# Performance work log

Hardware: AMD Instinct MI355X
Metric: run time of the kernel (lower is better)

Reference implementation:

```python
import jax, jax.numpy as jnp
import numpy as np


def setup_inputs() -> dict:
    key = jax.random.key(0)
    kx, kb, kc, ka, kd = jax.random.split(key, 5)
    B, L, D, N = 8, 4096, 1024, 128
    x = jax.random.normal(kx, (B, L, D), jnp.float32)
    B_w = jax.random.normal(kb, (N, D), jnp.float32) * 0.01  # nn.Linear(d_model->d_state).weight
    C_w = jax.random.normal(kc, (D, N), jnp.float32)         # nn.Linear(d_state->d_model).weight
    # stable negative log_A (HiPPO init gives -|diag|+0.1 < 0)
    log_A = -jax.random.uniform(ka, (N,), jnp.float32) * 3.0 - 0.1
    D_param = jax.random.normal(kd, (D,), jnp.float32)
    return dict(x=x, B_w=B_w, C_w=C_w, log_A=log_A, D_param=D_param)


def reference(x, B_w, C_w, log_A, D_param):
    # x: (B,L,D); B_w: (N,D); C_w: (D,N); log_A: (N,); D_param: (D,)
    A = jnp.exp(log_A)                                   # (N,) diagonal transition
    x_proj = jnp.einsum('bld,nd->bln', x, B_w)           # B @ x  -> (B,L,N)

    def step(h, u):                                      # h_t = A*h_{t-1} + u_t
        h = A * h + u
        return h, h

    h0 = jnp.zeros((x.shape[0], B_w.shape[0]), x.dtype)  # (B,N)
    _, hs = jax.lax.scan(step, h0, jnp.swapaxes(x_proj, 0, 1))  # hs: (L,B,N)

    y = jnp.einsum('lbn,dn->bld', hs, C_w)               # C @ h -> (B,L,D)
    y = y + x * D_param                                  # skip term D*x

    last = x_proj[:, -1, :]                              # (B,N)
    final_state = jnp.broadcast_to(last.mean(axis=0, keepdims=True), last.shape)
    return y, final_state
```

## Files before the change

### kernel.cpp

```cpp
#include <hip/hip_runtime.h>


typedef _Float16 half8 __attribute__((ext_vector_type(8)));
typedef _Float16 half4 __attribute__((ext_vector_type(4)));
typedef float f32x4 __attribute__((ext_vector_type(4)));

#define BDIM 8
#define LDIM 4096
#define DDIM 1024
#define NDIM 128
#define MTOT (BDIM * LDIM)
#define CHUNK 32
#define NCHUNK (LDIM / CHUNK)
#define TOTCHUNK (BDIM * NCHUNK)

__device__ __forceinline__ void dma16(const void* g, void* l) {
    __builtin_amdgcn_global_load_lds((const __attribute__((address_space(1))) void*)g,
                                     (__attribute__((address_space(3))) void*)l, 16, 0, 0);
}

__global__ __launch_bounds__(256) void prep(const float* __restrict__ x,
                                            const float* __restrict__ Bw,
                                            const float* __restrict__ Cw,
                                            _Float16* __restrict__ Bwh,
                                            _Float16* __restrict__ Cwh,
                                            float* __restrict__ out) {
    const int blk = blockIdx.x;
    const int t = threadIdx.x;
    if (blk < 128) {
        const int n = blk;
        float s = 0.f;
        const float* br = Bw + n * DDIM;
        for (int b = 0; b < BDIM; ++b) {
            const float* xr = x + ((size_t)b * LDIM + (LDIM - 1)) * DDIM;
            for (int k = t; k < DDIM; k += 256)
                s = fmaf(xr[k], br[k], s);
        }
        __shared__ float red[256];
        red[t] = s;
        __syncthreads();
        for (int off = 128; off > 0; off >>= 1) {
            if (t < off) red[t] += red[t + off];
            __syncthreads();
        }
        if (t == 0) {
            float v = red[0] * 0.125f;
            for (int b = 0; b < BDIM; ++b)
                out[(size_t)MTOT * DDIM + b * NDIM + n] = v;
        }
    } else {
        const int base = (blk - 128) * 4096;
#pragma unroll
        for (int j = 0; j < 4; ++j) {
            int e = base + j * 1024 + t * 4;
            const float* src;
            _Float16* dst;
            if (e < 131072) { src = Bw + e; dst = Bwh + e; }
            else            { src = Cw + (e - 131072); dst = Cwh + (e - 131072); }
            float4 v = *reinterpret_cast<const float4*>(src);
            half4 h = { (_Float16)v.x, (_Float16)v.y, (_Float16)v.z, (_Float16)v.w };
            *reinterpret_cast<half4*>(dst) = h;
        }
    }
}

__global__ __launch_bounds__(256, 8) void gemm1(const float* __restrict__ x,
                                                const _Float16* __restrict__ Bwh,
                                                const float* __restrict__ logA,
                                                float* __restrict__ xp,
                                                float* __restrict__ agg) {
    __shared__ _Float16 As[32 * 64];
    __shared__ _Float16 Bs[128 * 64];
    const int t = threadIdx.x;
    const int row0 = blockIdx.x * 32;
    const int wave = t >> 6, lane = t & 63;
    const int wr = (wave >> 1) * 16, wc = (wave & 1) * 64;
    const int lrow = lane & 15, kq = (lane >> 4) * 8;
    const int kc = kq >> 3;

    f32x4 acc[4] = {};

    for (int kk = 0; kk < DDIM; kk += 64) {
#pragma unroll
        for (int inst = 0; inst < 4; ++inst) {
            int s = inst * 256 + t;
            int r = s >> 3;
            int cs = (s & 7) ^ (r & 7);
            dma16(&Bwh[(size_t)r * DDIM + kk + cs * 8], &Bs[(inst * 256 + wave * 64) * 8]);
        }
#pragma unroll
        for (int j = 0; j < 2; ++j) {
            int s = t + 256 * j;
            int r = s >> 4, c4 = s & 15;
            float4 v = *reinterpret_cast<const float4*>(&x[(size_t)(row0 + r) * DDIM + kk + c4 * 4]);
            half4 h = { (_Float16)v.x, (_Float16)v.y, (_Float16)v.z, (_Float16)v.w };
            int pc = (c4 >> 1) ^ (r & 7);
            *reinterpret_cast<half4*>(&As[r * 64 + pc * 8 + (c4 & 1) * 4]) = h;
        }
        __syncthreads();

        const int arow = wr + lrow;
#pragma unroll
        for (int ks = 0; ks < 2; ++ks) {
            half8 af = *reinterpret_cast<const half8*>(&As[arow * 64 + ((ks * 4 + kc) ^ (arow & 7)) * 8]);
            half8 bf[4];
#pragma unroll
            for (int ct = 0; ct < 4; ++ct) {
                int brow = wc + ct * 16 + lrow;
                bf[ct] = *reinterpret_cast<const half8*>(&Bs[brow * 64 + ((ks * 4 + kc) ^ (brow & 7)) * 8]);
            }
#pragma unroll
            for (int ct = 0; ct < 4; ++ct)
                acc[ct] = __builtin_amdgcn_mfma_f32_16x16x32_f16(af, bf[ct], acc[ct], 0, 0, 0);
        }
        __syncthreads();
    }

    float* tb = (float*)Bs;
    const int q4 = (lane >> 4) * 4;
#pragma unroll
    for (int ct = 0; ct < 4; ++ct) {
        int col = wc + ct * 16 + lrow;
#pragma unroll
        for (int i = 0; i < 4; ++i)
            tb[(wr + q4 + i) * NDIM + col] = acc[ct][i];
    }
    __syncthreads();
#pragma unroll
    for (int j = 0; j < 4; ++j) {
        int idx = t + 256 * j;
        int row = idx >> 5, c4 = idx & 31;
        *reinterpret_cast<float4*>(&xp[(size_t)(row0 + row) * NDIM + c4 * 4]) =
            *reinterpret_cast<const float4*>(&tb[row * NDIM + c4 * 4]);
    }
    if (t < 128) {
        const float A = expf(logA[t]);
        float h = 0.f;
#pragma unroll
        for (int j = 0; j < CHUNK; ++j)
            h = fmaf(A, h, tb[j * NDIM + t]);
        agg[(size_t)blockIdx.x * NDIM + t] = h;
    }
}

__global__ void scan_carry(const float* __restrict__ agg, const float* __restrict__ logA,
                           float* __restrict__ hprev) {
    const int idx = blockIdx.x * blockDim.x + threadIdx.x;
    const int b = idx >> 7, n = idx & 127;
    const float Ac = expf((float)CHUNK * logA[n]);
    float c = 0.f;
#pragma unroll 8
    for (int ch = 0; ch < NCHUNK; ++ch) {
        int g = (b * NCHUNK + ch) * NDIM + n;
        hprev[g] = c;
        c = fmaf(Ac, c, agg[g]);
    }
}

__global__ void scan_final(const float* __restrict__ xp, const float* __restrict__ logA,
                           const float* __restrict__ hprev, _Float16* __restrict__ hs) {
    const int chunk = blockIdx.x;
    const int n = threadIdx.x;
    const float A = expf(logA[n]);
    float h = hprev[chunk * NDIM + n];
    const float* u = xp + (size_t)chunk * CHUNK * NDIM + n;
    _Float16* o = hs + (size_t)chunk * CHUNK * NDIM + n;
#pragma unroll
    for (int j = 0; j < CHUNK; ++j) {
        h = fmaf(A, h, u[j * NDIM]);
        o[j * NDIM] = (_Float16)h;
    }
}

#define SBUFW 132
__global__ __launch_bounds__(256, 6) void gemm2(const _Float16* __restrict__ hs,
                                                const _Float16* __restrict__ Cwh,
                                                const float* __restrict__ x,
                                                const float* __restrict__ Dp,
                                                float* __restrict__ y) {
    __shared__ __align__(16) _Float16 hsP[64 * 128];
    __shared__ __align__(16) float DpS[128];

    const int t = threadIdx.x;
    const int id = blockIdx.x;
    const int xb = (id & 7) * 64 + ((id >> 3) & 63);
    const int yb = id >> 9;
    const int row0 = xb * 64;
    const int col0 = yb * 128;
    const int wave = t >> 6, lane = t & 63;
    const int wr = wave * 16;
    const int lrow = lane & 15, kq = (lane >> 4) * 8;

    if (t < 128) DpS[t] = Dp[col0 + t];

#pragma unroll
    for (int inst = 0; inst < 4; ++inst) {
        int s = inst * 256 + t;
        int r = s >> 4, c = s & 15;
        dma16(&hs[(size_t)(row0 + r) * NDIM + ((c ^ (r & 7)) * 8)],
              &hsP[(inst * 256 + wave * 64) * 8]);
    }
    __syncthreads();

    const _Float16* cb = Cwh + (size_t)(col0 + lrow) * NDIM + kq;
    const int ar = wr + lrow;

    f32x4 acc[8] = {};
#pragma unroll 1
    for (int kb = 0; kb < 4; ++kb) {
        int ck = kb * 4 + (kq >> 3);
        half8 af = *reinterpret_cast<const half8*>(&hsP[ar * NDIM + ((ck ^ (ar & 7)) * 8)]);
#pragma unroll
        for (int ct = 0; ct < 8; ++ct) {
            half8 bf = *reinterpret_cast<const half8*>(cb + (size_t)ct * 16 * NDIM + kb * 32);
            acc[ct] = __builtin_amdgcn_mfma_f32_16x16x32_f16(af, bf, acc[ct], 0, 0, 0);
        }
    }

    float* buf = (float*)hsP;
    const int q4 = (lane >> 4) * 4;
#pragma unroll 1
    for (int s = 0; s < 4; ++s) {
        __syncthreads();
        if (wave == s) {
#pragma unroll
            for (int ct = 0; ct < 8; ++ct) {
                int col = ct * 16 + lrow;
#pragma unroll
                for (int i = 0; i < 4; ++i)
                    buf[(q4 + i) * SBUFW + col] = acc[ct][i];
            }
        }
        __syncthreads();
#pragma unroll
        for (int j = 0; j < 2; ++j) {
            int idx = t + 256 * j;
            int row = idx >> 5, c4 = idx & 31;
            int grow = row0 + s * 16 + row;
            float4 a = *reinterpret_cast<const float4*>(&buf[row * SBUFW + c4 * 4]);
            float4 xv = *reinterpret_cast<const float4*>(&x[(size_t)grow * DDIM + col0 + c4 * 4]);
            float4 dp = *reinterpret_cast<const float4*>(&DpS[c4 * 4]);
            float4 o;
            o.x = a.x + xv.x * dp.x;
            o.y = a.y + xv.y * dp.y;
            o.z = a.z + xv.z * dp.z;
            o.w = a.w + xv.w * dp.w;
            *reinterpret_cast<float4*>(&y[(size_t)grow * DDIM + col0 + c4 * 4]) = o;
        }
    }
}

extern "C" void kernel_launch(void* const* d_in, const int* in_sizes, int n_in,
                              void* d_out, int out_size, void* d_ws, size_t ws_size,
                              hipStream_t stream) {
    const float* x    = (const float*)d_in[0];
    const float* Bw   = (const float*)d_in[1];
    const float* Cw   = (const float*)d_in[2];
    const float* logA = (const float*)d_in[3];
    const float* Dp   = (const float*)d_in[4];
    float* out = (float*)d_out;

    char* ws = (char*)d_ws;
    float*    xp    = (float*)   (ws);
    _Float16* hs    = (_Float16*)(ws + 16777216);
    float*    agg   = (float*)   (ws + 25165824);
    float*    hprev = (float*)   (ws + 25690112);
    _Float16* Bwh   = (_Float16*)(ws + 26214400);
    _Float16* Cwh   = (_Float16*)(ws + 26476544);

    prep<<<192, 256, 0, stream>>>(x, Bw, Cw, Bwh, Cwh, out);
    gemm1<<<MTOT / 32, 256, 0, stream>>>(x, Bwh, logA, xp, agg);
    scan_carry<<<8, 128, 0, stream>>>(agg, logA, hprev);
    scan_final<<<TOTCHUNK, 128, 0, stream>>>(xp, logA, hprev, hs);
    gemm2<<<4096, 256, 0, stream>>>(hs, Cwh, x, Dp, out);
}
```

Measured before the change: 357.7 us.

## Prefetch x tile into LDS via async DMA and store the epilogue in one pass

The gemm2 kernel now issues the x tile for the skip term as global-to-LDS DMA loads alongside the hs tile, before the MFMA loop, so that read overlaps with setup instead of sitting in the epilogue. The D*x term is folded into the accumulators in registers. All four waves then write their results to LDS together and store y after a single barrier pair, replacing the four-step serialized staging. Shared memory grows to 48 KB, the occupancy hint drops from 6 to 3 blocks, and the k loop is fully unrolled, which cuts concurrency and may raise register pressure.

```diff
diff --git a/kernel.cpp b/kernel.cpp
--- a/kernel.cpp
+++ b/kernel.cpp
@@ -172,14 +172,14 @@
     }
 }
 
-#define SBUFW 132
-__global__ __launch_bounds__(256, 6) void gemm2(const _Float16* __restrict__ hs,
+__global__ __launch_bounds__(256, 3) void gemm2(const _Float16* __restrict__ hs,
                                                 const _Float16* __restrict__ Cwh,
                                                 const float* __restrict__ x,
                                                 const float* __restrict__ Dp,
                                                 float* __restrict__ y) {
-    __shared__ __align__(16) _Float16 hsP[64 * 128];
-    __shared__ __align__(16) float DpS[128];
+    __shared__ __align__(16) char smem[49152];
+    _Float16* hsP = (_Float16*)smem;
+    float* xS = (float*)(smem + 16384);
 
     const int t = threadIdx.x;
     const int id = blockIdx.x;
@@ -191,8 +191,6 @@
     const int wr = wave * 16;
     const int lrow = lane & 15, kq = (lane >> 4) * 8;
 
-    if (t < 128) DpS[t] = Dp[col0 + t];
-
 #pragma unroll
     for (int inst = 0; inst < 4; ++inst) {
         int s = inst * 256 + t;
@@ -200,13 +198,20 @@
         dma16(&hs[(size_t)(row0 + r) * NDIM + ((c ^ (r & 7)) * 8)],
               &hsP[(inst * 256 + wave * 64) * 8]);
     }
+#pragma unroll
+    for (int inst = 0; inst < 8; ++inst) {
+        int slab = wave * 8 + inst;
+        int r = slab * 2 + (lane >> 5);
+        int c = lane & 31;
+        dma16(&x[(size_t)(row0 + r) * DDIM + col0 + c * 4], &xS[slab * 256]);
+    }
     __syncthreads();
 
     const _Float16* cb = Cwh + (size_t)(col0 + lrow) * NDIM + kq;
     const int ar = wr + lrow;
 
     f32x4 acc[8] = {};
-#pragma unroll 1
+#pragma unroll
     for (int kb = 0; kb < 4; ++kb) {
         int ck = kb * 4 + (kq >> 3);
         half8 af = *reinterpret_cast<const half8*>(&hsP[ar * NDIM + ((ck ^ (ar & 7)) * 8)]);
@@ -217,36 +222,31 @@
         }
     }
 
-    float* buf = (float*)hsP;
     const int q4 = (lane >> 4) * 4;
-#pragma unroll 1
-    for (int s = 0; s < 4; ++s) {
-        __syncthreads();
-        if (wave == s) {
-#pragma unroll
-            for (int ct = 0; ct < 8; ++ct) {
-                int col = ct * 16 + lrow;
-#pragma unroll
-                for (int i = 0; i < 4; ++i)
-                    buf[(q4 + i) * SBUFW + col] = acc[ct][i];
-            }
-        }
-        __syncthreads();
-#pragma unroll
-        for (int j = 0; j < 2; ++j) {
-            int idx = t + 256 * j;
-            int row = idx >> 5, c4 = idx & 31;
-            int grow = row0 + s * 16 + row;
-            float4 a = *reinterpret_cast<const float4*>(&buf[row * SBUFW + c4 * 4]);
-            float4 xv = *reinterpret_cast<const float4*>(&x[(size_t)grow * DDIM + col0 + c4 * 4]);
-            float4 dp = *reinterpret_cast<const float4*>(&DpS[c4 * 4]);
-            float4 o;
-            o.x = a.x + xv.x * dp.x;
-            o.y = a.y + xv.y * dp.y;
-            o.z = a.z + xv.z * dp.z;
-            o.w = a.w + xv.w * dp.w;
-            *reinterpret_cast<float4*>(&y[(size_t)grow * DDIM + col0 + c4 * 4]) = o;
-        }
+    float dp[8];
+#pragma unroll
+    for (int ct = 0; ct < 8; ++ct) dp[ct] = Dp[col0 + ct * 16 + lrow];
+#pragma unroll
+    for (int ct = 0; ct < 8; ++ct)
+#pragma unroll
+        for (int i = 0; i < 4; ++i)
+            acc[ct][i] = fmaf(xS[(wr + q4 + i) * NDIM + ct * 16 + lrow], dp[ct], acc[ct][i]);
+
+    __syncthreads();
+    float* buf = (float*)smem;
+#pragma unroll
+    for (int ct = 0; ct < 8; ++ct)
+#pragma unroll
+        for (int i = 0; i < 4; ++i)
+            buf[wave * 2112 + (q4 + i) * 132 + ct * 16 + lrow] = acc[ct][i];
+    __syncthreads();
+#pragma unroll
+    for (int j = 0; j < 8; ++j) {
+        int idx = t + 256 * j;
+        int row = idx >> 5, c4 = idx & 31;
+        float4 v = *reinterpret_cast<const float4*>(
+            &buf[(row >> 4) * 2112 + (row & 15) * 132 + c4 * 4]);
+        *reinterpret_cast<float4*>(&y[(size_t)(row0 + row) * DDIM + col0 + c4 * 4]) = v;
     }
 }
 
```

Measured after the change: 352.2 us. Within noise of the previous version (-1.5%).
